# Optimization experiments

Hardware: AMD Instinct MI355X
Metric: run time of the kernel (lower is better)

Reference implementation:

```python
import jax, jax.numpy as jnp
import numpy as np

B = 32          # batch size
N_IN = 1000000  # dofs of source function space (CG1 mesh)
N_OUT = 500000  # number of evaluation points (DG0 on VertexOnlyMesh)
K = 3           # nonzeros per row (CG1 barycentric interpolation)


def setup_inputs() -> dict:
    key = jax.random.key(0)
    k1, k2, k3 = jax.random.split(key, 3)
    x = jax.random.normal(k1, (B, N_IN), dtype=jnp.float32)
    # barycentric-style weights: nonnegative, rows sum to 1
    w_raw = jax.random.uniform(k2, (N_OUT, K), dtype=jnp.float32)
    w = w_raw / jnp.sum(w_raw, axis=1, keepdims=True)
    idx = jax.random.randint(k3, (N_OUT, K), 0, N_IN, dtype=jnp.int32)
    return {"x": x, "w": w, "idx": idx}


def reference(x, w, idx):
    # y = A @ x^T per sample, with A the sparse interpolation operator:
    # y[b, o] = sum_k w[o, k] * x[b, idx[o, k]]
    gathered = x[:, idx]                      # [B, N_OUT, K] gather
    return jnp.einsum("ok,bok->bo", w, gathered)  # [B, N_OUT]
```

## Files before the change

kernel.cpp:

```cpp
#include <hip/hip_runtime.h>
#include <hip/hip_bf16.h>

#define B_DIM 32
#define N_IN 1000000
#define N_OUT 500000

typedef float nfloat4 __attribute__((ext_vector_type(4)));

__device__ __forceinline__ unsigned int f32_to_bf16_rne(float f) {
    unsigned int u = __float_as_uint(f);
    unsigned int rounding = 0x7fffu + ((u >> 16) & 1u);
    return (u + rounding) >> 16;
}

__global__ __launch_bounds__(256) void transpose_bf16_kernel(
    const float* __restrict__ x, unsigned short* __restrict__ xT)
{
    __shared__ unsigned int tile[64][17];
    const int t  = threadIdx.x;
    const int i0 = blockIdx.x * 64;

    const int qi = t & 15;
    const int p  = t >> 4;

    const float* r0 = x + (size_t)(2 * p)     * N_IN + i0 + qi * 4;
    const float* r1 = x + (size_t)(2 * p + 1) * N_IN + i0 + qi * 4;
    const nfloat4 va = __builtin_nontemporal_load((const nfloat4*)r0);
    const nfloat4 vb = __builtin_nontemporal_load((const nfloat4*)r1);

    tile[qi * 4 + 0][p] = f32_to_bf16_rne(va.x) | (f32_to_bf16_rne(vb.x) << 16);
    tile[qi * 4 + 1][p] = f32_to_bf16_rne(va.y) | (f32_to_bf16_rne(vb.y) << 16);
    tile[qi * 4 + 2][p] = f32_to_bf16_rne(va.z) | (f32_to_bf16_rne(vb.z) << 16);
    tile[qi * 4 + 3][p] = f32_to_bf16_rne(va.w) | (f32_to_bf16_rne(vb.w) << 16);
    __syncthreads();

    const int ii = t >> 2;
    const int g  = t & 3;
    uint4 pk;
    pk.x = tile[ii][g * 4 + 0];
    pk.y = tile[ii][g * 4 + 1];
    pk.z = tile[ii][g * 4 + 2];
    pk.w = tile[ii][g * 4 + 3];
    *(uint4*)((char*)xT + (size_t)(i0 + ii) * 64 + g * 16) = pk;
}

__global__ __launch_bounds__(256) void gather_bf16_v2_kernel(
    const unsigned short* __restrict__ xT,
    const float* __restrict__ w,
    const int*   __restrict__ idx,
    float* __restrict__ out)
{
    const int t = threadIdx.x;
    const int g = t >> 2;
    const int l = t & 3;
    const int o = blockIdx.x * 64 + g;
    if (o >= N_OUT) return;

    const int base = 3 * o;
    const int   i0 = __builtin_nontemporal_load(idx + base + 0);
    const int   i1 = __builtin_nontemporal_load(idx + base + 1);
    const int   i2 = __builtin_nontemporal_load(idx + base + 2);
    const float w0 = __builtin_nontemporal_load(w + base + 0);
    const float w1 = __builtin_nontemporal_load(w + base + 1);
    const float w2 = __builtin_nontemporal_load(w + base + 2);

    const uint4 v0 = *(const uint4*)(xT + (size_t)i0 * B_DIM + l * 8);
    const uint4 v1 = *(const uint4*)(xT + (size_t)i1 * B_DIM + l * 8);
    const uint4 v2 = *(const uint4*)(xT + (size_t)i2 * B_DIM + l * 8);

    float acc[8];
#pragma unroll
    for (int j = 0; j < 8; ++j) acc[j] = 0.0f;

    const unsigned int u0[4] = {v0.x, v0.y, v0.z, v0.w};
    const unsigned int u1[4] = {v1.x, v1.y, v1.z, v1.w};
    const unsigned int u2[4] = {v2.x, v2.y, v2.z, v2.w};
#pragma unroll
    for (int m = 0; m < 4; ++m) {
        float a = acc[2 * m], c = acc[2 * m + 1];
        a = fmaf(w0, __uint_as_float(u0[m] << 16), a);
        c = fmaf(w0, __uint_as_float(u0[m] & 0xffff0000u), c);
        a = fmaf(w1, __uint_as_float(u1[m] << 16), a);
        c = fmaf(w1, __uint_as_float(u1[m] & 0xffff0000u), c);
        a = fmaf(w2, __uint_as_float(u2[m] << 16), a);
        c = fmaf(w2, __uint_as_float(u2[m] & 0xffff0000u), c);
        acc[2 * m] = a; acc[2 * m + 1] = c;
    }

    float* obase = out + (size_t)(8 * l) * N_OUT + o;
#pragma unroll
    for (int j = 0; j < 8; ++j) {
        __builtin_nontemporal_store(acc[j], obase + (size_t)j * N_OUT);
    }
}

__global__ __launch_bounds__(256) void direct_kernel(
    const float* __restrict__ x,
    const float* __restrict__ w,
    const int*   __restrict__ idx,
    float* __restrict__ out)
{
    const int o = blockIdx.x * blockDim.x + threadIdx.x;
    if (o >= N_OUT) return;
    const int base = 3 * o;
    const int i0 = idx[base + 0], i1 = idx[base + 1], i2 = idx[base + 2];
    const float w0 = w[base + 0], w1 = w[base + 1], w2 = w[base + 2];
#pragma unroll 4
    for (int b = 0; b < B_DIM; ++b) {
        const float* __restrict__ xr = x + (size_t)b * N_IN;
        float acc = w0 * xr[i0];
        acc = fmaf(w1, xr[i1], acc);
        acc = fmaf(w2, xr[i2], acc);
        out[(size_t)b * N_OUT + o] = acc;
    }
}

extern "C" void kernel_launch(void* const* d_in, const int* in_sizes, int n_in,
                              void* d_out, int out_size, void* d_ws, size_t ws_size,
                              hipStream_t stream) {
    const float* x   = (const float*)d_in[0];
    const float* w   = (const float*)d_in[1];
    const int*   idx = (const int*)d_in[2];
    float* out = (float*)d_out;

    const size_t xt_bytes = (size_t)N_IN * B_DIM * sizeof(unsigned short);

    if (ws_size >= xt_bytes) {
        unsigned short* xT = (unsigned short*)d_ws;
        transpose_bf16_kernel<<<N_IN / 64, 256, 0, stream>>>(x, xT);
        const int blocks = (N_OUT + 63) / 64;
        gather_bf16_v2_kernel<<<blocks, 256, 0, stream>>>(xT, w, idx, out);
    } else {
        const int blocks = (N_OUT + 255) / 256;
        direct_kernel<<<blocks, 256, 0, stream>>>(x, w, idx, out);
    }
}
```

Before: 248.0 us.

## Fuse transpose and gather into one persistent cooperative kernel with grid sync

```diff
diff --git a/kernel.cpp b/kernel.cpp
--- a/kernel.cpp
+++ b/kernel.cpp
@@ -1,9 +1,14 @@
 #include <hip/hip_runtime.h>
 #include <hip/hip_bf16.h>
+#include <hip/hip_cooperative_groups.h>
+
+namespace cg = cooperative_groups;
 
 #define B_DIM 32
 #define N_IN 1000000
 #define N_OUT 500000
+#define NTILES_T (N_IN / 64)
+#define NTILES_G ((N_OUT + 63) / 64)
 
 typedef float nfloat4 __attribute__((ext_vector_type(4)));
 
@@ -13,15 +18,13 @@
     return (u + rounding) >> 16;
 }
 
-__global__ __launch_bounds__(256) void transpose_bf16_kernel(
-    const float* __restrict__ x, unsigned short* __restrict__ xT)
-{
-    __shared__ unsigned int tile[64][17];
-    const int t  = threadIdx.x;
-    const int i0 = blockIdx.x * 64;
-
+__device__ __forceinline__ void transpose_tile_body(
+    const float* __restrict__ x, unsigned short* __restrict__ xT,
+    unsigned int (*tile)[17], const int t, const int tb)
+{
     const int qi = t & 15;
     const int p  = t >> 4;
+    const int i0 = tb * 64;
 
     const float* r0 = x + (size_t)(2 * p)     * N_IN + i0 + qi * 4;
     const float* r1 = x + (size_t)(2 * p + 1) * N_IN + i0 + qi * 4;
@@ -35,25 +38,23 @@
     __syncthreads();
 
     const int ii = t >> 2;
-    const int g  = t & 3;
+    const int gq = t & 3;
     uint4 pk;
-    pk.x = tile[ii][g * 4 + 0];
-    pk.y = tile[ii][g * 4 + 1];
-    pk.z = tile[ii][g * 4 + 2];
-    pk.w = tile[ii][g * 4 + 3];
-    *(uint4*)((char*)xT + (size_t)(i0 + ii) * 64 + g * 16) = pk;
-}
-
-__global__ __launch_bounds__(256) void gather_bf16_v2_kernel(
-    const unsigned short* __restrict__ xT,
-    const float* __restrict__ w,
-    const int*   __restrict__ idx,
-    float* __restrict__ out)
-{
-    const int t = threadIdx.x;
+    pk.x = tile[ii][gq * 4 + 0];
+    pk.y = tile[ii][gq * 4 + 1];
+    pk.z = tile[ii][gq * 4 + 2];
+    pk.w = tile[ii][gq * 4 + 3];
+    *(uint4*)((char*)xT + (size_t)(i0 + ii) * 64 + gq * 16) = pk;
+}
+
+__device__ __forceinline__ void gather_tile_body(
+    const unsigned short* __restrict__ xT, const float* __restrict__ w,
+    const int* __restrict__ idx, float* __restrict__ out,
+    const int t, const int ob)
+{
     const int g = t >> 2;
     const int l = t & 3;
-    const int o = blockIdx.x * 64 + g;
+    const int o = ob * 64 + g;
     if (o >= N_OUT) return;
 
     const int base = 3 * o;
@@ -94,11 +95,53 @@
     }
 }
 
+__global__ __launch_bounds__(256, 8) void fused_kernel(
+    const float* __restrict__ x, const float* __restrict__ w,
+    const int* __restrict__ idx, float* __restrict__ out,
+    unsigned short* __restrict__ xT)
+{
+    __shared__ unsigned int tile[64][17];
+    const int t = threadIdx.x;
+
+    {
+        const int tpb = (NTILES_T + gridDim.x - 1) / gridDim.x;
+        const int ts  = blockIdx.x * tpb;
+        const int te  = (ts + tpb < NTILES_T) ? (ts + tpb) : NTILES_T;
+        for (int tb = ts; tb < te; ++tb) {
+            transpose_tile_body(x, xT, tile, t, tb);
+            __syncthreads();
+        }
+    }
+
+    cg::this_grid().sync();
+
+    {
+        const int gpb = (NTILES_G + gridDim.x - 1) / gridDim.x;
+        const int os  = blockIdx.x * gpb;
+        const int oe  = (os + gpb < NTILES_G) ? (os + gpb) : NTILES_G;
+        for (int ob = os; ob < oe; ++ob) {
+            gather_tile_body(xT, w, idx, out, t, ob);
+        }
+    }
+}
+
+__global__ __launch_bounds__(256) void transpose_bf16_kernel(
+    const float* __restrict__ x, unsigned short* __restrict__ xT)
+{
+    __shared__ unsigned int tile[64][17];
+    transpose_tile_body(x, xT, tile, threadIdx.x, blockIdx.x);
+}
+
+__global__ __launch_bounds__(256) void gather_bf16_v2_kernel(
+    const unsigned short* __restrict__ xT, const float* __restrict__ w,
+    const int* __restrict__ idx, float* __restrict__ out)
+{
+    gather_tile_body(xT, w, idx, out, threadIdx.x, blockIdx.x);
+}
+
 __global__ __launch_bounds__(256) void direct_kernel(
-    const float* __restrict__ x,
-    const float* __restrict__ w,
-    const int*   __restrict__ idx,
-    float* __restrict__ out)
+    const float* __restrict__ x, const float* __restrict__ w,
+    const int* __restrict__ idx, float* __restrict__ out)
 {
     const int o = blockIdx.x * blockDim.x + threadIdx.x;
     if (o >= N_OUT) return;
@@ -127,9 +170,35 @@
 
     if (ws_size >= xt_bytes) {
         unsigned short* xT = (unsigned short*)d_ws;
-        transpose_bf16_kernel<<<N_IN / 64, 256, 0, stream>>>(x, xT);
-        const int blocks = (N_OUT + 63) / 64;
-        gather_bf16_v2_kernel<<<blocks, 256, 0, stream>>>(xT, w, idx, out);
+
+        static int coop_grid = -2;
+        if (coop_grid == -2) {
+            int nb = 0;
+            if (hipOccupancyMaxActiveBlocksPerMultiprocessor(
+                    &nb, fused_kernel, 256, 0) == hipSuccess && nb > 0) {
+                long g = (long)nb * 256;
+                if (g > 2048) g = 2048;
+                coop_grid = (int)g;
+            } else {
+                coop_grid = 0;
+            }
+        }
+
+        bool done = false;
+        if (coop_grid > 0) {
+            void* args[] = {(void*)&x, (void*)&w, (void*)&idx, (void*)&out, (void*)&xT};
+            hipError_t e = hipLaunchCooperativeKernel(
+                fused_kernel, dim3(coop_grid), dim3(256), args, 0, stream);
+            if (e == hipSuccess) {
+                done = true;
+            } else {
+                coop_grid = 0;
+            }
+        }
+        if (!done) {
+            transpose_bf16_kernel<<<N_IN / 64, 256, 0, stream>>>(x, xT);
+            gather_bf16_v2_kernel<<<NTILES_G, 256, 0, stream>>>(xT, w, idx, out);
+        }
     } else {
         const int blocks = (N_OUT + 255) / 256;
         direct_kernel<<<blocks, 256, 0, stream>>>(x, w, idx, out);
```

New measurement: 378.5 us. 1.53x slower.
